# Performance work log

Hardware: AMD Instinct MI355X
Metric: run time of the kernel (lower is better)

## Reference

```python
import jax, jax.numpy as jnp
import numpy as np

V = 128000  # output_size (vocab)
H = 1024    # hidden_size


def setup_inputs() -> dict:
    key = jax.random.key(0)
    ks = jax.random.split(key, 9)
    s = 1.0 / np.sqrt(H)
    return {
        "input_token": jax.random.randint(ks[0], (1,), 0, V, dtype=jnp.int64)
        if jax.config.jax_enable_x64 else jax.random.randint(ks[0], (1,), 0, V, dtype=jnp.int32),
        "hidden": jax.random.normal(ks[1], (1, 1, H), dtype=jnp.float32),
        "emb": jax.random.normal(ks[2], (V, H), dtype=jnp.float32),
        "w_ih": jax.random.normal(ks[3], (3 * H, H), dtype=jnp.float32) * s,
        "w_hh": jax.random.normal(ks[4], (3 * H, H), dtype=jnp.float32) * s,
        "b_ih": jax.random.normal(ks[5], (3 * H,), dtype=jnp.float32) * s,
        "b_hh": jax.random.normal(ks[6], (3 * H,), dtype=jnp.float32) * s,
        "w_out": jax.random.normal(ks[7], (V, H), dtype=jnp.float32) * s,
        "b_out": jax.random.normal(ks[8], (V,), dtype=jnp.float32) * s,
    }


def gru_step(x, h, w_ih, w_hh, b_ih, b_hh):
    # x, h: [1, H]; weights: [3H, H] with PyTorch gate order (r, z, n)
    gi = x @ w_ih.T + b_ih            # [1, 3H]
    gh = h @ w_hh.T + b_hh            # [1, 3H]
    i_r, i_z, i_n = jnp.split(gi, 3, axis=-1)
    h_r, h_z, h_n = jnp.split(gh, 3, axis=-1)
    r = jax.nn.sigmoid(i_r + h_r)
    z = jax.nn.sigmoid(i_z + h_z)
    n = jnp.tanh(i_n + r * h_n)
    return (1.0 - z) * n + z * h      # [1, H]


def reference(input_token, hidden, emb, w_ih, w_hh, b_ih, b_hh, w_out, b_out):
    # Embedding lookup -> [1, 1, H]; dropout is identity (eval mode)
    x = emb[input_token].reshape(1, 1, H)
    h_new = gru_step(x[0], hidden[0], w_ih, w_hh, b_ih, b_hh)  # [1, H]
    logits = h_new @ w_out.T + b_out                           # [1, V]
    log_probs = jax.nn.log_softmax(logits, axis=1)
    return log_probs, h_new[None, :, :]  # ([1, V], [1, 1, H])
```

## Files before the change

### kernel.cpp

```cpp
#include <hip/hip_runtime.h>
#include <math.h>

#define V 128000
#define H 1024
#define H3 3072

typedef float f32x4 __attribute__((ext_vector_type(4)));

#define GI_OFF 0
#define GH_OFF 3072
#define ROWS_PER_BLK 16
#define NBLK3 (V / ROWS_PER_BLK)
#define PART_OFF 6144
#define RED_OFF (PART_OFF + 2 * NBLK3)

#define R_CACHED 48000

__device__ __forceinline__ float wave_reduce_sum(float v) {
#pragma unroll
    for (int off = 32; off > 0; off >>= 1)
        v += __shfl_xor(v, off, 64);
    return v;
}

__global__ __launch_bounds__(256) void k_gates(
    const int* __restrict__ token_p, const float* __restrict__ hidden,
    const float* __restrict__ emb,
    const float* __restrict__ w_ih, const float* __restrict__ w_hh,
    const float* __restrict__ b_ih, const float* __restrict__ b_hh,
    float* __restrict__ ws)
{
    const int gwave = (int)((blockIdx.x * blockDim.x + threadIdx.x) >> 6);
    const int lane  = threadIdx.x & 63;
    if (gwave >= 2 * H3) return;

    const float* w;
    const float* vec;
    float bias;
    float* out;
    if (gwave < H3) {
        const int row = gwave;
        w    = w_ih + (size_t)row * H;
        vec  = emb + (size_t)token_p[0] * H;
        bias = b_ih[row];
        out  = ws + GI_OFF + row;
    } else {
        const int row = gwave - H3;
        w    = w_hh + (size_t)row * H;
        vec  = hidden;
        bias = b_hh[row];
        out  = ws + GH_OFF + row;
    }

    const f32x4* w4 = (const f32x4*)w;
    const f32x4* v4 = (const f32x4*)vec;
    float acc = 0.f;
#pragma unroll
    for (int it = 0; it < 4; ++it) {
        f32x4 a = w4[it * 64 + lane];
        f32x4 b = v4[it * 64 + lane];
        acc = fmaf(a.x, b.x, acc);
        acc = fmaf(a.y, b.y, acc);
        acc = fmaf(a.z, b.z, acc);
        acc = fmaf(a.w, b.w, acc);
    }
    acc = wave_reduce_sum(acc);
    if (lane == 0) *out = acc + bias;
}

__global__ __launch_bounds__(256) void k_combine(
    const float* __restrict__ hidden, const float* __restrict__ ws,
    float* __restrict__ d_out)
{
    const int k = blockIdx.x * blockDim.x + threadIdx.x;
    if (k >= H) return;
    const float gr  = ws[GI_OFF + k]         + ws[GH_OFF + k];
    const float gz  = ws[GI_OFF + H + k]     + ws[GH_OFF + H + k];
    const float gin = ws[GI_OFF + 2 * H + k];
    const float ghn = ws[GH_OFF + 2 * H + k];
    const float r = 1.f / (1.f + expf(-gr));
    const float z = 1.f / (1.f + expf(-gz));
    const float n = tanhf(gin + r * ghn);
    d_out[V + k] = (1.f - z) * n + z * hidden[k];
}

__global__ __launch_bounds__(256) void k_logits(
    const float* __restrict__ w_out, const float* __restrict__ b_out,
    float* __restrict__ d_out, float* __restrict__ ws)
{
    __shared__ float sl[ROWS_PER_BLK];
    const int wave = threadIdx.x >> 6;
    const int lane = threadIdx.x & 63;

    const f32x4* h4p = (const f32x4*)(d_out + V);
    f32x4 h4[4];
#pragma unroll
    for (int it = 0; it < 4; ++it) h4[it] = h4p[it * 64 + lane];

    const int base_row = blockIdx.x * ROWS_PER_BLK + wave * 4;
    float acc[4] = {0.f, 0.f, 0.f, 0.f};

    if (base_row + 3 < R_CACHED) {
#pragma unroll
        for (int i = 0; i < 4; ++i) {
            const f32x4* w4 = (const f32x4*)(w_out + (size_t)(base_row + i) * H);
#pragma unroll
            for (int it = 0; it < 4; ++it) {
                f32x4 a = w4[it * 64 + lane];
                acc[i] = fmaf(a.x, h4[it].x, acc[i]);
                acc[i] = fmaf(a.y, h4[it].y, acc[i]);
                acc[i] = fmaf(a.z, h4[it].z, acc[i]);
                acc[i] = fmaf(a.w, h4[it].w, acc[i]);
            }
        }
    } else {
#pragma unroll
        for (int i = 0; i < 4; ++i) {
            const f32x4* w4 = (const f32x4*)(w_out + (size_t)(base_row + i) * H);
#pragma unroll
            for (int it = 0; it < 4; ++it) {
                f32x4 a = __builtin_nontemporal_load(w4 + it * 64 + lane);
                acc[i] = fmaf(a.x, h4[it].x, acc[i]);
                acc[i] = fmaf(a.y, h4[it].y, acc[i]);
                acc[i] = fmaf(a.z, h4[it].z, acc[i]);
                acc[i] = fmaf(a.w, h4[it].w, acc[i]);
            }
        }
    }

#pragma unroll
    for (int i = 0; i < 4; ++i) {
        const float r = wave_reduce_sum(acc[i]);
        if (lane == 0) {
            const float l = r + b_out[base_row + i];
            d_out[base_row + i] = l;
            sl[wave * 4 + i] = l;
        }
    }
    __syncthreads();
    if (threadIdx.x == 0) {
        float m = sl[0];
#pragma unroll
        for (int i = 1; i < ROWS_PER_BLK; ++i) m = fmaxf(m, sl[i]);
        float s = 0.f;
#pragma unroll
        for (int i = 0; i < ROWS_PER_BLK; ++i) s += expf(sl[i] - m);
        ws[PART_OFF + 2 * blockIdx.x]     = m;
        ws[PART_OFF + 2 * blockIdx.x + 1] = s;
    }
}

__global__ __launch_bounds__(1024) void k_reduce(float* __restrict__ ws)
{
    __shared__ float sm[1024], ss[1024];
    const int t = threadIdx.x;
    float m = -INFINITY, s = 0.f;
    for (int i = t; i < NBLK3; i += 1024) {
        const float m2 = ws[PART_OFF + 2 * i];
        const float s2 = ws[PART_OFF + 2 * i + 1];
        if (m2 > m) { s = s * expf(m - m2) + s2; m = m2; }
        else        { s += s2 * expf(m2 - m); }
    }
    sm[t] = m; ss[t] = s;
    __syncthreads();
    for (int off = 512; off > 0; off >>= 1) {
        if (t < off) {
            float m2 = sm[t + off], s2 = ss[t + off];
            float mm = sm[t],       sc = ss[t];
            if (m2 > mm) { sc = sc * expf(mm - m2) + s2; mm = m2; }
            else         { sc += s2 * expf(m2 - mm); }
            sm[t] = mm; ss[t] = sc;
        }
        __syncthreads();
    }
    if (t == 0) ws[RED_OFF] = sm[0] + logf(ss[0]);
}

__global__ __launch_bounds__(256) void k_final(
    float* __restrict__ d_out, const float* __restrict__ ws)
{
    const int i = blockIdx.x * blockDim.x + threadIdx.x;
    if (i < V) d_out[i] -= ws[RED_OFF];
}

extern "C" void kernel_launch(void* const* d_in, const int* in_sizes, int n_in,
                              void* d_out_v, int out_size, void* d_ws, size_t ws_size,
                              hipStream_t stream) {
    const int*   token  = (const int*)d_in[0];
    const float* hidden = (const float*)d_in[1];
    const float* emb    = (const float*)d_in[2];
    const float* w_ih   = (const float*)d_in[3];
    const float* w_hh   = (const float*)d_in[4];
    const float* b_ih   = (const float*)d_in[5];
    const float* b_hh   = (const float*)d_in[6];
    const float* w_out  = (const float*)d_in[7];
    const float* b_out  = (const float*)d_in[8];
    float* d_out = (float*)d_out_v;
    float* ws    = (float*)d_ws;

    k_gates  <<<(2 * H3) / 4, 256, 0, stream>>>(token, hidden, emb, w_ih, w_hh, b_ih, b_hh, ws);
    k_combine<<<(H + 255) / 256, 256, 0, stream>>>(hidden, ws, d_out);
    k_logits <<<NBLK3, 256, 0, stream>>>(w_out, b_out, d_out, ws);
    k_reduce <<<1, 1024, 0, stream>>>(ws);
    k_final  <<<(V + 255) / 256, 256, 0, stream>>>(d_out, ws);
}
```

Baseline: 98.58 us.

## Fuse GRU gate and combine kernels, merge softmax reduce into final pass

```diff
diff --git a/kernel.cpp b/kernel.cpp
--- a/kernel.cpp
+++ b/kernel.cpp
@@ -3,16 +3,12 @@
 
 #define V 128000
 #define H 1024
-#define H3 3072
 
 typedef float f32x4 __attribute__((ext_vector_type(4)));
 
-#define GI_OFF 0
-#define GH_OFF 3072
 #define ROWS_PER_BLK 16
 #define NBLK3 (V / ROWS_PER_BLK)
-#define PART_OFF 6144
-#define RED_OFF (PART_OFF + 2 * NBLK3)
+
 
 #define R_CACHED 48000
 
@@ -23,33 +19,31 @@
     return v;
 }
 
-__global__ __launch_bounds__(256) void k_gates(
+__global__ __launch_bounds__(384) void k_gates_combine(
     const int* __restrict__ token_p, const float* __restrict__ hidden,
     const float* __restrict__ emb,
     const float* __restrict__ w_ih, const float* __restrict__ w_hh,
     const float* __restrict__ b_ih, const float* __restrict__ b_hh,
-    float* __restrict__ ws)
+    float* __restrict__ d_out)
 {
-    const int gwave = (int)((blockIdx.x * blockDim.x + threadIdx.x) >> 6);
-    const int lane  = threadIdx.x & 63;
-    if (gwave >= 2 * H3) return;
+    __shared__ float g[6];
+    const int k    = blockIdx.x;
+    const int wave = threadIdx.x >> 6;
+    const int lane = threadIdx.x & 63;
 
     const float* w;
     const float* vec;
     float bias;
-    float* out;
-    if (gwave < H3) {
-        const int row = gwave;
+    if (wave < 3) {
+        const int row = wave * H + k;
         w    = w_ih + (size_t)row * H;
         vec  = emb + (size_t)token_p[0] * H;
         bias = b_ih[row];
-        out  = ws + GI_OFF + row;
     } else {
-        const int row = gwave - H3;
+        const int row = (wave - 3) * H + k;
         w    = w_hh + (size_t)row * H;
         vec  = hidden;
         bias = b_hh[row];
-        out  = ws + GH_OFF + row;
     }
 
     const f32x4* w4 = (const f32x4*)w;
@@ -65,23 +59,15 @@
         acc = fmaf(a.w, b.w, acc);
     }
     acc = wave_reduce_sum(acc);
-    if (lane == 0) *out = acc + bias;
-}
+    if (lane == 0) g[wave] = acc + bias;
+    __syncthreads();
 
-__global__ __launch_bounds__(256) void k_combine(
-    const float* __restrict__ hidden, const float* __restrict__ ws,
-    float* __restrict__ d_out)
-{
-    const int k = blockIdx.x * blockDim.x + threadIdx.x;
-    if (k >= H) return;
-    const float gr  = ws[GI_OFF + k]         + ws[GH_OFF + k];
-    const float gz  = ws[GI_OFF + H + k]     + ws[GH_OFF + H + k];
-    const float gin = ws[GI_OFF + 2 * H + k];
-    const float ghn = ws[GH_OFF + 2 * H + k];
-    const float r = 1.f / (1.f + expf(-gr));
-    const float z = 1.f / (1.f + expf(-gz));
-    const float n = tanhf(gin + r * ghn);
-    d_out[V + k] = (1.f - z) * n + z * hidden[k];
+    if (threadIdx.x == 0) {
+        const float r = 1.f / (1.f + expf(-(g[0] + g[3])));
+        const float z = 1.f / (1.f + expf(-(g[1] + g[4])));
+        const float n = tanhf(g[2] + r * g[5]);
+        d_out[V + k] = (1.f - z) * n + z * hidden[k];
+    }
 }
 
 __global__ __launch_bounds__(256) void k_logits(
@@ -145,42 +131,47 @@
         float s = 0.f;
 #pragma unroll
         for (int i = 0; i < ROWS_PER_BLK; ++i) s += expf(sl[i] - m);
-        ws[PART_OFF + 2 * blockIdx.x]     = m;
-        ws[PART_OFF + 2 * blockIdx.x + 1] = s;
+        ws[2 * blockIdx.x]     = m;
+        ws[2 * blockIdx.x + 1] = s;
     }
 }
 
-__global__ __launch_bounds__(1024) void k_reduce(float* __restrict__ ws)
+__global__ __launch_bounds__(256) void k_final(
+    float* __restrict__ d_out, const float* __restrict__ ws)
 {
-    __shared__ float sm[1024], ss[1024];
+    __shared__ float sm[256], ss[256];
+    __shared__ float sC;
     const int t = threadIdx.x;
+
     float m = -INFINITY, s = 0.f;
-    for (int i = t; i < NBLK3; i += 1024) {
-        const float m2 = ws[PART_OFF + 2 * i];
-        const float s2 = ws[PART_OFF + 2 * i + 1];
+    for (int j = t; j < NBLK3; j += 256) {
+        const float m2 = ws[2 * j];
+        const float s2 = ws[2 * j + 1];
         if (m2 > m) { s = s * expf(m - m2) + s2; m = m2; }
         else        { s += s2 * expf(m2 - m); }
     }
     sm[t] = m; ss[t] = s;
     __syncthreads();
-    for (int off = 512; off > 0; off >>= 1) {
+#pragma unroll
+    for (int off = 128; off > 0; off >>= 1) {
         if (t < off) {
-            float m2 = sm[t + off], s2 = ss[t + off];
-            float mm = sm[t],       sc = ss[t];
+            const float m2 = sm[t + off], s2 = ss[t + off];
+            float mm = sm[t], sc = ss[t];
             if (m2 > mm) { sc = sc * expf(mm - m2) + s2; mm = m2; }
             else         { sc += s2 * expf(m2 - mm); }
             sm[t] = mm; ss[t] = sc;
         }
         __syncthreads();
     }
-    if (t == 0) ws[RED_OFF] = sm[0] + logf(ss[0]);
-}
+    if (t == 0) sC = sm[0] + logf(ss[0]);
+    __syncthreads();
 
-__global__ __launch_bounds__(256) void k_final(
-    float* __restrict__ d_out, const float* __restrict__ ws)
-{
-    const int i = blockIdx.x * blockDim.x + threadIdx.x;
-    if (i < V) d_out[i] -= ws[RED_OFF];
+    const float C = sC;
+    f32x4* o4 = (f32x4*)d_out;
+    const int i = blockIdx.x * 256 + t;
+    f32x4 v = o4[i];
+    v.x -= C; v.y -= C; v.z -= C; v.w -= C;
+    o4[i] = v;
 }
 
 extern "C" void kernel_launch(void* const* d_in, const int* in_sizes, int n_in,
@@ -198,9 +189,7 @@
     float* d_out = (float*)d_out_v;
     float* ws    = (float*)d_ws;
 
-    k_gates  <<<(2 * H3) / 4, 256, 0, stream>>>(token, hidden, emb, w_ih, w_hh, b_ih, b_hh, ws);
-    k_combine<<<(H + 255) / 256, 256, 0, stream>>>(hidden, ws, d_out);
-    k_logits <<<NBLK3, 256, 0, stream>>>(w_out, b_out, d_out, ws);
-    k_reduce <<<1, 1024, 0, stream>>>(ws);
-    k_final  <<<(V + 255) / 256, 256, 0, stream>>>(d_out, ws);
+    k_gates_combine<<<H, 384, 0, stream>>>(token, hidden, emb, w_ih, w_hh, b_ih, b_hh, d_out);
+    k_logits       <<<NBLK3, 256, 0, stream>>>(w_out, b_out, d_out, ws);
+    k_final        <<<V / 4 / 256, 256, 0, stream>>>(d_out, ws);
 }
```

Measured after the change: 103.1 us. 4.6% more time.
